# Performance work log

Hardware: AMD Instinct MI355X
Metric: run time of the kernel (lower is better)

Reference implementation:

```python
import jax, jax.numpy as jnp
import numpy as np

EMB = 128
N_TEXT = 80000
N_NODES = 100000
E = 800000
N_REL = 500
PRED_IN = 4 * EMB + 2 * 2 + 2 * 2 * (2 + 2)  # 532


def scatter_mean(x, src, dst, num_nodes):
    # PyG MessagePassing(aggr='mean'): mean of x[src] grouped by dst; empty groups -> 0
    sums = jax.ops.segment_sum(x[src], dst, num_segments=num_nodes)
    cnt = jax.ops.segment_sum(jnp.ones((src.shape[0], 1), x.dtype), dst, num_segments=num_nodes)
    return sums / jnp.maximum(cnt, 1.0)


def setup_inputs() -> dict:
    key = jax.random.key(0)
    ks = jax.random.split(key, 12)
    inp = {
        "h_id_tensor": jax.random.randint(ks[0], (E,), 0, N_NODES),
        "r_id_tensor": jax.random.randint(ks[1], (E,), 0, N_REL),
        "t_id_tensor": jax.random.randint(ks[2], (E,), 0, N_NODES),
        "q_emb": jax.random.normal(ks[3], (1, EMB), jnp.float32),
        "entity_embs": jax.random.normal(ks[4], (N_TEXT, EMB), jnp.float32),
        "num_non_text_entities": N_NODES - N_TEXT,
        "relation_embs": jax.random.normal(ks[5], (N_REL, EMB), jnp.float32),
        "topic_entity_one_hot": jax.random.uniform(ks[6], (N_NODES, 2), jnp.float32),
        # learned params
        "non_text_emb": jax.random.normal(ks[7], (1, EMB), jnp.float32) * 0.02,
        "W1": jax.random.normal(ks[8], (EMB, PRED_IN), jnp.float32) / np.sqrt(PRED_IN),
        "b1": jnp.zeros((EMB,), jnp.float32),
        "W2": jax.random.normal(ks[9], (1, EMB), jnp.float32) / np.sqrt(EMB),
        "b2": jnp.zeros((1,), jnp.float32),
    }
    return inp


def reference(h_id_tensor, r_id_tensor, t_id_tensor, q_emb, entity_embs,
              num_non_text_entities, relation_embs, topic_entity_one_hot,
              non_text_emb, W1, b1, W2, b2):
    num_nodes = entity_embs.shape[0] + num_non_text_entities
    # node embeddings: text entities + shared non-text embedding row
    h_e = jnp.concatenate(
        [entity_embs, jnp.broadcast_to(non_text_emb, (num_non_text_entities, EMB))], axis=0)

    # DDE: forward rounds over (h->t), reverse rounds over (t->h); scatter-mean diffusion
    dde_list = []
    h_pe = topic_entity_one_hot
    for _ in range(2):
        h_pe = scatter_mean(h_pe, h_id_tensor, t_id_tensor, num_nodes)
        dde_list.append(h_pe)
    h_pe_rev = topic_entity_one_hot
    for _ in range(2):
        h_pe_rev = scatter_mean(h_pe_rev, t_id_tensor, h_id_tensor, num_nodes)
        dde_list.append(h_pe_rev)

    h_e_full = jnp.concatenate([h_e, topic_entity_one_hot] + dde_list, axis=1)  # [N, EMB+10]

    h_r = relation_embs[r_id_tensor]                       # [E, EMB]
    h_q = jnp.broadcast_to(q_emb, (h_r.shape[0], EMB))     # [E, EMB]
    h_triple = jnp.concatenate(
        [h_q, h_e_full[h_id_tensor], h_r, h_e_full[t_id_tensor]], axis=1)  # [E, PRED_IN]

    hidden = jax.nn.relu(h_triple @ W1.T + b1)             # [E, EMB]
    pred = hidden @ W2.T + b2                              # [E, 1]
    return pred
```

## Files before the change

kernel.cpp:

```cpp
#include <hip/hip_runtime.h>

#define EMB 128
#define W1LD 532
#define KP 160
#define ST 264
#define BSH 9
#define BNODES 512
#define EPB 8192

typedef unsigned long long u64;
typedef unsigned int u32;
typedef unsigned short u16;
typedef __attribute__((ext_vector_type(8))) short short8;
typedef __attribute__((ext_vector_type(4))) float f32x4;

__device__ __forceinline__ u16 f2bf(float x) {
    unsigned u = __float_as_uint(x);
    unsigned r = (u + 0x7fffu + ((u >> 16) & 1u)) >> 16;
    return (u16)r;
}
__device__ __forceinline__ float bf2f_lo(unsigned u) { return __uint_as_float(u << 16); }
__device__ __forceinline__ float bf2f_hi(unsigned u) { return __uint_as_float(u & 0xffff0000u); }

__global__ __launch_bounds__(1024) void khist(
    const int* __restrict__ h_id, const int* __restrict__ t_id,
    u32* __restrict__ hist, int E, int NBKT, int NSB)
{
    __shared__ u32 lh[512];
    const int t = threadIdx.x, sb = blockIdx.x;
    const int rows = 2 * NBKT;
    if (t < rows) lh[t] = 0;
    __syncthreads();
    const int base = sb * EPB;
#pragma unroll
    for (int c = 0; c < EPB / 1024; c++) {
        int e = base + c * 1024 + t;
        if (e < E) {
            atomicAdd(&lh[t_id[e] >> BSH], 1u);
            atomicAdd(&lh[NBKT + (h_id[e] >> BSH)], 1u);
        }
    }
    __syncthreads();
    if (t < rows) hist[t * NSB + sb] = lh[t];
}

__global__ __launch_bounds__(256) void kscanA(
    u32* __restrict__ hist, u32* __restrict__ tot, int NSB)
{
    __shared__ u32 s[256];
    const int t = threadIdx.x, row = blockIdx.x;
    u32 v = (t < NSB) ? hist[row * NSB + t] : 0;
    s[t] = v;
    __syncthreads();
    for (int o = 1; o < 256; o <<= 1) {
        u32 x = (t >= o) ? s[t - o] : 0;
        __syncthreads();
        s[t] += x;
        __syncthreads();
    }
    if (t < NSB) hist[row * NSB + t] = s[t] - v;
    if (t == 255) tot[row] = s[255];
}

__global__ __launch_bounds__(1024) void kplace(
    const int* __restrict__ h_id, const int* __restrict__ t_id,
    const u32* __restrict__ hist, const u32* __restrict__ tot,
    u32* __restrict__ bstart,
    u32* __restrict__ perm_t, u32* __restrict__ perm_h,
    int E, int NBKT, int NSB)
{
    __shared__ u32 cur[512];
    const int t = threadIdx.x, sb = blockIdx.x;
    const int rows = 2 * NBKT;
    if (t < rows) {
        const int d  = (t < NBKT) ? 1 : 0;
        const int b0 = (t < NBKT) ? 0 : NBKT;
        u32 base = 0;
        for (int b = b0; b < t; b++) base += tot[b];
        cur[t] = base + hist[t * NSB + sb];
        if (sb == 0) {
            const int seg = (t < NBKT) ? 0 : (NBKT + 1);
            bstart[seg + (t - b0)] = base;
            if (t == b0) bstart[seg + NBKT] = (u32)E;
        }
        (void)d;
    }
    __syncthreads();
    const int ebase = sb * EPB;
#pragma unroll
    for (int c = 0; c < EPB / 1024; c++) {
        int e = ebase + c * 1024 + t;
        if (e < E) {
            int tt = t_id[e], h = h_id[e];
            u32 pt = atomicAdd(&cur[tt >> BSH], 1u);
            perm_t[pt] = (u32)h | ((u32)(tt & (BNODES - 1)) << 17);
            u32 ph = atomicAdd(&cur[NBKT + (h >> BSH)], 1u);
            perm_h[ph] = (u32)tt | ((u32)(h & (BNODES - 1)) << 17);
        }
    }
}

template<int ROUND>
__global__ __launch_bounds__(256) void kscat(
    const u32* __restrict__ perm_t, const u32* __restrict__ perm_h,
    const u32* __restrict__ bstart,
    const float* __restrict__ topic,
    const float* __restrict__ src_t, const float* __restrict__ src_h,
    float* __restrict__ out_t, float* __restrict__ out_h,
    const float* __restrict__ W1, const float* __restrict__ q,
    const float* __restrict__ rel, const float* __restrict__ b1,
    u16* __restrict__ WBF, float* __restrict__ qWb, u16* __restrict__ Rbf,
    int N, int NBKT, int NREL)
{
    const int bid = blockIdx.x, t = threadIdx.x;
    if (bid < 2 * NBKT) {
        __shared__ u64 acc[BNODES];
        const int d = (bid < NBKT) ? 0 : 1;
        const int b = bid - d * NBKT;
        const u32* perm = d ? perm_h : perm_t;
        const float* srcv = (ROUND == 1) ? topic : (d ? src_h : src_t);
        float* out = d ? out_h : out_t;

        for (int i = t; i < BNODES; i += 256) acc[i] = 0;
        __syncthreads();
        const u32 s0 = bstart[d * (NBKT + 1) + b];
        const u32 s1 = bstart[d * (NBKT + 1) + b + 1];
        for (u32 i = s0 + t; i < s1; i += 256) {
            u32 rec  = perm[i];
            u32 src  = rec & 0x1FFFFu;
            u32 slot = rec >> 17;
            float2 v = *(const float2*)(srcv + 2 * src);
            u64 p = (u64)__float2uint_rn(v.x * 1048576.0f)
                  | ((u64)__float2uint_rn(v.y * 1048576.0f) << 26)
                  | (1ull << 52);
            atomicAdd(&acc[slot], p);
        }
        __syncthreads();
        for (int i = t; i < BNODES; i += 256) {
            int node = b * BNODES + i;
            if (node < N) {
                u64 a = acc[i];
                float cnt = (float)(u32)(a >> 52);
                float inv = (1.0f / 1048576.0f) / fmaxf(cnt, 1.0f);
                float2 m;
                m.x = (float)(u32)(a & 0x3FFFFFFu) * inv;
                m.y = (float)(u32)((a >> 26) & 0x3FFFFFFu) * inv;
                *(float2*)(out + 2 * node) = m;
            }
        }
        return;
    }
    if (ROUND != 1) return;
    const int pb = bid - 2 * NBKT;
    if (pb < KP) {
        int k = pb, n = t;
        float v = 0.0f;
        if (k < 138) {
            v = (n < 128) ? W1[(size_t)n * W1LD + 128 + k]
                          : W1[(size_t)(n - 128) * W1LD + 394 + k];
        }
        int kstep = k >> 5, quad = (k >> 3) & 3, j = k & 7;
        WBF[(((size_t)(kstep * 4 + quad) * 256 + n) << 3) + j] = f2bf(v);
        return;
    }
    int b = pb - KP;
    __shared__ float v[EMB];
    if (t < EMB) v[t] = (b == 0) ? q[t] : rel[(size_t)(b - 1) * EMB + t];
    __syncthreads();
    if (t < EMB) {
        const float* w = W1 + (size_t)t * W1LD + (b == 0 ? 0 : 266);
        float s = 0.0f;
#pragma unroll
        for (int k = 0; k < EMB; k += 4) {
            float4 wv = *(const float4*)(w + k);
            s += wv.x * v[k] + wv.y * v[k + 1] + wv.z * v[k + 2] + wv.w * v[k + 3];
        }
        if (b == 0) qWb[t] = s + b1[t];
        else        Rbf[(size_t)(b - 1) * EMB + t] = f2bf(s);
    }
}

__global__ __launch_bounds__(256) void k2b_node(
    const float* __restrict__ ent, const float* __restrict__ nte,
    const float* __restrict__ topic,
    const float* __restrict__ dde1f, const float* __restrict__ dde2f,
    const float* __restrict__ dde3f, const float* __restrict__ dde4f,
    const u16* __restrict__ WBF, const float* __restrict__ qWb,
    u16* __restrict__ A, u16* __restrict__ B,
    int NT, int N)
{
    __shared__ __align__(16) u16 lds[32 * ST];
    const int t = threadIdx.x;
    const int lane = t & 63;
    const int w    = t >> 6;
    const int ln15 = lane & 15;
    const int quad = lane >> 4;
    const int m0   = (w & 1) * 16;
    const int n0   = (w >> 1) * 128;
    const int nblk = blockIdx.x * 32;

    {
        int m  = t >> 3;
        int kq = (t & 7) << 4;
        int gn = nblk + m;
        const float* src = (gn < N) ? ((gn < NT) ? ent + (size_t)gn * EMB + kq
                                                 : nte + kq)
                                    : nte;
        u16 pk[16];
#pragma unroll
        for (int p = 0; p < 4; p++) {
            float4 v = (gn < N) ? *(const float4*)(src + 4 * p)
                                : make_float4(0.f, 0.f, 0.f, 0.f);
            pk[4 * p + 0] = f2bf(v.x); pk[4 * p + 1] = f2bf(v.y);
            pk[4 * p + 2] = f2bf(v.z); pk[4 * p + 3] = f2bf(v.w);
        }
        *(uint4*)&lds[m * ST + kq]     = *(uint4*)&pk[0];
        *(uint4*)&lds[m * ST + kq + 8] = *(uint4*)&pk[8];
    }
    if (t < 32) {
        int gn = nblk + t;
        if (gn < N) {
            float2 tp = *(const float2*)(topic + 2 * gn);
            float2 d1 = *(const float2*)(dde1f + 2 * gn);
            float2 d2 = *(const float2*)(dde2f + 2 * gn);
            float2 d3 = *(const float2*)(dde3f + 2 * gn);
            float2 d4 = *(const float2*)(dde4f + 2 * gn);
            lds[t * ST + 128] = f2bf(tp.x); lds[t * ST + 129] = f2bf(tp.y);
            lds[t * ST + 130] = f2bf(d1.x); lds[t * ST + 131] = f2bf(d1.y);
            lds[t * ST + 132] = f2bf(d2.x); lds[t * ST + 133] = f2bf(d2.y);
            lds[t * ST + 134] = f2bf(d3.x); lds[t * ST + 135] = f2bf(d3.y);
            lds[t * ST + 136] = f2bf(d4.x); lds[t * ST + 137] = f2bf(d4.y);
        } else {
#pragma unroll
            for (int z = 128; z < 138; z++) lds[t * ST + z] = 0;
        }
#pragma unroll
        for (int z = 138; z < KP; z++) lds[t * ST + z] = 0;
    }
    __syncthreads();

    f32x4 acc[8];
#pragma unroll
    for (int i = 0; i < 8; i++) acc[i] = (f32x4){0.f, 0.f, 0.f, 0.f};

    const u16* wbbase = WBF + (((size_t)quad * 256 + n0 + ln15) << 3);
#pragma unroll
    for (int ks = 0; ks < 5; ks++) {
        short8 a = *(const short8*)&lds[(m0 + ln15) * ST + ks * 32 + quad * 8];
        const u16* wb = wbbase + ((size_t)ks * 4 * 256 * 8);
#pragma unroll
        for (int nt = 0; nt < 8; nt++) {
            short8 b = *(const short8*)(wb + (nt << 7));
            acc[nt] = __builtin_amdgcn_mfma_f32_16x16x32_bf16(a, b, acc[nt], 0, 0, 0);
        }
    }

    __syncthreads();
#pragma unroll
    for (int nt = 0; nt < 8; nt++) {
        int c = n0 + nt * 16 + ln15;
        float qv = (n0 == 0) ? qWb[c] : 0.0f;
#pragma unroll
        for (int r = 0; r < 4; r++) {
            int row = m0 + quad * 4 + r;
            lds[row * ST + c] = f2bf(acc[nt][r] + qv);
        }
    }
    __syncthreads();
    {
        int m  = t >> 3;
        int c0 = (t & 7) * 32;
        int gn = nblk + m;
        if (gn < N) {
            uint4 v0 = *(uint4*)&lds[m * ST + c0];
            uint4 v1 = *(uint4*)&lds[m * ST + c0 + 8];
            uint4 v2 = *(uint4*)&lds[m * ST + c0 + 16];
            uint4 v3 = *(uint4*)&lds[m * ST + c0 + 24];
            u16* dst = (c0 < 128) ? (A + (size_t)gn * EMB + c0)
                                  : (B + (size_t)gn * EMB + (c0 - 128));
            ((uint4*)dst)[0] = v0;
            ((uint4*)dst)[1] = v1;
            ((uint4*)dst)[2] = v2;
            ((uint4*)dst)[3] = v3;
        }
    }
}

__global__ __launch_bounds__(256) void edge_pred(
    const int* __restrict__ h_id, const int* __restrict__ r_id,
    const int* __restrict__ t_id,
    const u16* __restrict__ A, const u16* __restrict__ B,
    const u16* __restrict__ Rbf,
    const float* __restrict__ W2, const float* __restrict__ b2,
    float* __restrict__ out, int E)
{
    const int t    = threadIdx.x;
    const int lane = t & 63;
    const int g    = lane >> 4;
    const int k    = lane & 15;
    const int wv   = t >> 6;
    const int e    = blockIdx.x * 16 + wv * 4 + g;

    const float4 w0 = *(const float4*)(W2 + k * 8);
    const float4 w1 = *(const float4*)(W2 + k * 8 + 4);

    float s = 0.0f;
    if (e < E) {
        const int h = h_id[e], r = r_id[e], tt = t_id[e];
        const uint4 ua = *(const uint4*)(A + (size_t)h * EMB + k * 8);
        const uint4 ub = *(const uint4*)(B + (size_t)tt * EMB + k * 8);
        const uint4 ur = *(const uint4*)(Rbf + (size_t)r * EMB + k * 8);

        s  = fmaxf(bf2f_lo(ua.x) + bf2f_lo(ur.x) + bf2f_lo(ub.x), 0.0f) * w0.x;
        s += fmaxf(bf2f_hi(ua.x) + bf2f_hi(ur.x) + bf2f_hi(ub.x), 0.0f) * w0.y;
        s += fmaxf(bf2f_lo(ua.y) + bf2f_lo(ur.y) + bf2f_lo(ub.y), 0.0f) * w0.z;
        s += fmaxf(bf2f_hi(ua.y) + bf2f_hi(ur.y) + bf2f_hi(ub.y), 0.0f) * w0.w;
        s += fmaxf(bf2f_lo(ua.z) + bf2f_lo(ur.z) + bf2f_lo(ub.z), 0.0f) * w1.x;
        s += fmaxf(bf2f_hi(ua.z) + bf2f_hi(ur.z) + bf2f_hi(ub.z), 0.0f) * w1.y;
        s += fmaxf(bf2f_lo(ua.w) + bf2f_lo(ur.w) + bf2f_lo(ub.w), 0.0f) * w1.z;
        s += fmaxf(bf2f_hi(ua.w) + bf2f_hi(ur.w) + bf2f_hi(ub.w), 0.0f) * w1.w;
    }
    s += __shfl_xor(s, 1, 64);
    s += __shfl_xor(s, 2, 64);
    s += __shfl_xor(s, 4, 64);
    s += __shfl_xor(s, 8, 64);
    if (k == 0 && e < E) out[e] = s + b2[0];
}


extern "C" void kernel_launch(void* const* d_in, const int* in_sizes, int n_in,
                              void* d_out, int out_size, void* d_ws, size_t ws_size,
                              hipStream_t stream)
{
    const int*   h_id  = (const int*)d_in[0];
    const int*   r_id  = (const int*)d_in[1];
    const int*   t_id  = (const int*)d_in[2];
    const float* q_emb = (const float*)d_in[3];
    const float* ent   = (const float*)d_in[4];
    const float* rel   = (const float*)d_in[6];
    const float* topic = (const float*)d_in[7];
    const float* nte   = (const float*)d_in[8];
    const float* W1    = (const float*)d_in[9];
    const float* b1    = (const float*)d_in[10];
    const float* W2    = (const float*)d_in[11];
    const float* b2    = (const float*)d_in[12];

    const int E    = in_sizes[0];
    const int NT   = in_sizes[4] / EMB;
    const int N    = in_sizes[7] / 2;
    const int NREL = in_sizes[6] / EMB;

    const int NBKT = (N + BNODES - 1) >> BSH;
    const int NSB  = (E + EPB - 1) / EPB;

    float* qWb  = (float*)d_ws;
    u16* Rbf    = (u16*)(qWb + EMB);
    u16* WBF    = Rbf + (size_t)NREL * EMB;
    float* dde1f = (float*)(WBF + (size_t)KP * 256);
    float* dde2f = dde1f + 2 * (size_t)N;
    float* dde3f = dde2f + 2 * (size_t)N;
    float* dde4f = dde3f + 2 * (size_t)N;
    u16* Aw = (u16*)(dde4f + 2 * (size_t)N);
    u16* Bw = Aw + (size_t)N * EMB;

    u32* hist   = (u32*)Aw;
    u32* tot    = hist + (size_t)2 * NBKT * NSB;
    u32* bstart = tot + 2 * NBKT;
    u32* perm_t = bstart + 2 * (NBKT + 1);
    u32* perm_h = perm_t + E;

    const int nn = (N + 31) / 32;

    khist<<<NSB, 1024, 0, stream>>>(h_id, t_id, hist, E, NBKT, NSB);
    kscanA<<<2 * NBKT, 256, 0, stream>>>(hist, tot, NSB);
    kplace<<<NSB, 1024, 0, stream>>>(h_id, t_id, hist, tot, bstart,
                                     perm_t, perm_h, E, NBKT, NSB);

    kscat<1><<<2 * NBKT + KP + 1 + NREL, 256, 0, stream>>>(
        perm_t, perm_h, bstart, topic, nullptr, nullptr, dde1f, dde3f,
        W1, q_emb, rel, b1, WBF, qWb, Rbf, N, NBKT, NREL);

    kscat<2><<<2 * NBKT, 256, 0, stream>>>(
        perm_t, perm_h, bstart, topic, dde1f, dde3f, dde2f, dde4f,
        W1, q_emb, rel, b1, WBF, qWb, Rbf, N, NBKT, NREL);

    k2b_node<<<nn, 256, 0, stream>>>(
        ent, nte, topic, dde1f, dde2f, dde3f, dde4f,
        WBF, qWb, Aw, Bw, NT, N);

    edge_pred<<<(E + 15) / 16, 256, 0, stream>>>(
        h_id, r_id, t_id, Aw, Bw, Rbf, W2, b2, (float*)d_out, E);
}
```

Baseline: 256.3 us.

## Process edges in head-sorted order with packed records and fp16 dot2 epilogue

The placement kernel now writes a 64-bit packed record (h, t, r, original edge id) in head-bucket order, and the edge prediction kernel reads these sorted records. Consecutive edges then share A rows, which improves cache locality, and results are scattered back to their original index. Node and relation projections switch from bf16 to fp16 so the edge epilogue can use packed half adds, max and fdot2. EPB is also halved to get more histogram and placement blocks. Costs are wider perm records, a scattered output write, fp16 range and precision risk, and a fallback path when workspace or size limits fail.

```diff
diff --git a/kernel.cpp b/kernel.cpp
--- a/kernel.cpp
+++ b/kernel.cpp
@@ -6,21 +6,49 @@
 #define ST 264
 #define BSH 9
 #define BNODES 512
-#define EPB 8192
+#define EPB 4096
 
 typedef unsigned long long u64;
 typedef unsigned int u32;
 typedef unsigned short u16;
 typedef __attribute__((ext_vector_type(8))) short short8;
 typedef __attribute__((ext_vector_type(4))) float f32x4;
+typedef _Float16 h2 __attribute__((ext_vector_type(2)));
 
 __device__ __forceinline__ u16 f2bf(float x) {
     unsigned u = __float_as_uint(x);
     unsigned r = (u + 0x7fffu + ((u >> 16) & 1u)) >> 16;
     return (u16)r;
 }
-__device__ __forceinline__ float bf2f_lo(unsigned u) { return __uint_as_float(u << 16); }
-__device__ __forceinline__ float bf2f_hi(unsigned u) { return __uint_as_float(u & 0xffff0000u); }
+__device__ __forceinline__ u16 f2h(float x) {
+    union { _Float16 h; u16 u; } c; c.h = (_Float16)x; return c.u;
+}
+__device__ __forceinline__ h2 u2h(unsigned u) {
+    union { unsigned u; h2 h; } c; c.u = u; return c.h;
+}
+
+__device__ __forceinline__ float ep8(const uint4& ua, const uint4& ub,
+                                     const uint4& ur, const uint4& uw, float s) {
+    const h2 z = {(_Float16)0.0f, (_Float16)0.0f};
+#define EP1(c)                                                         \
+    {                                                                  \
+        h2 x = u2h(ua.c) + u2h(ur.c) + u2h(ub.c);                      \
+        x = __builtin_elementwise_max(x, z);                           \
+        h2 w = u2h(uw.c);                                              \
+        _Pragma("clang diagnostic push")                               \
+        s = FDOT2(x, w, s);                                            \
+        _Pragma("clang diagnostic pop")                                \
+    }
+#if __has_builtin(__builtin_amdgcn_fdot2)
+#define FDOT2(x, w, s) __builtin_amdgcn_fdot2(x, w, s, false)
+#else
+#define FDOT2(x, w, s) (s + (float)x[0] * (float)w[0] + (float)x[1] * (float)w[1])
+#endif
+    EP1(x) EP1(y) EP1(z) EP1(w)
+#undef EP1
+#undef FDOT2
+    return s;
+}
 
 __global__ __launch_bounds__(1024) void khist(
     const int* __restrict__ h_id, const int* __restrict__ t_id,
@@ -63,17 +91,17 @@
 }
 
 __global__ __launch_bounds__(1024) void kplace(
-    const int* __restrict__ h_id, const int* __restrict__ t_id,
+    const int* __restrict__ h_id, const int* __restrict__ r_id,
+    const int* __restrict__ t_id,
     const u32* __restrict__ hist, const u32* __restrict__ tot,
     u32* __restrict__ bstart,
-    u32* __restrict__ perm_t, u32* __restrict__ perm_h,
+    u32* __restrict__ perm_t, u64* __restrict__ perm_e,
     int E, int NBKT, int NSB)
 {
     __shared__ u32 cur[512];
     const int t = threadIdx.x, sb = blockIdx.x;
     const int rows = 2 * NBKT;
     if (t < rows) {
-        const int d  = (t < NBKT) ? 1 : 0;
         const int b0 = (t < NBKT) ? 0 : NBKT;
         u32 base = 0;
         for (int b = b0; b < t; b++) base += tot[b];
@@ -83,7 +111,6 @@
             bstart[seg + (t - b0)] = base;
             if (t == b0) bstart[seg + NBKT] = (u32)E;
         }
-        (void)d;
     }
     __syncthreads();
     const int ebase = sb * EPB;
@@ -91,25 +118,28 @@
     for (int c = 0; c < EPB / 1024; c++) {
         int e = ebase + c * 1024 + t;
         if (e < E) {
-            int tt = t_id[e], h = h_id[e];
+            int tt = t_id[e], h = h_id[e], r = r_id[e];
             u32 pt = atomicAdd(&cur[tt >> BSH], 1u);
             perm_t[pt] = (u32)h | ((u32)(tt & (BNODES - 1)) << 17);
             u32 ph = atomicAdd(&cur[NBKT + (h >> BSH)], 1u);
-            perm_h[ph] = (u32)tt | ((u32)(h & (BNODES - 1)) << 17);
+            perm_e[ph] = (u64)h | ((u64)tt << 17) | ((u64)r << 34)
+                       | ((u64)e << 43);
         }
     }
 }
 
 template<int ROUND>
 __global__ __launch_bounds__(256) void kscat(
-    const u32* __restrict__ perm_t, const u32* __restrict__ perm_h,
+    const u32* __restrict__ perm_t, const u64* __restrict__ perm_e,
     const u32* __restrict__ bstart,
     const float* __restrict__ topic,
     const float* __restrict__ src_t, const float* __restrict__ src_h,
     float* __restrict__ out_t, float* __restrict__ out_h,
     const float* __restrict__ W1, const float* __restrict__ q,
     const float* __restrict__ rel, const float* __restrict__ b1,
-    u16* __restrict__ WBF, float* __restrict__ qWb, u16* __restrict__ Rbf,
+    const float* __restrict__ W2,
+    u16* __restrict__ WBF, float* __restrict__ qWb,
+    u16* __restrict__ W2h, u16* __restrict__ Rbf,
     int N, int NBKT, int NREL)
 {
     const int bid = blockIdx.x, t = threadIdx.x;
@@ -117,7 +147,6 @@
         __shared__ u64 acc[BNODES];
         const int d = (bid < NBKT) ? 0 : 1;
         const int b = bid - d * NBKT;
-        const u32* perm = d ? perm_h : perm_t;
         const float* srcv = (ROUND == 1) ? topic : (d ? src_h : src_t);
         float* out = d ? out_h : out_t;
 
@@ -125,15 +154,28 @@
         __syncthreads();
         const u32 s0 = bstart[d * (NBKT + 1) + b];
         const u32 s1 = bstart[d * (NBKT + 1) + b + 1];
-        for (u32 i = s0 + t; i < s1; i += 256) {
-            u32 rec  = perm[i];
-            u32 src  = rec & 0x1FFFFu;
-            u32 slot = rec >> 17;
-            float2 v = *(const float2*)(srcv + 2 * src);
-            u64 p = (u64)__float2uint_rn(v.x * 1048576.0f)
-                  | ((u64)__float2uint_rn(v.y * 1048576.0f) << 26)
-                  | (1ull << 52);
-            atomicAdd(&acc[slot], p);
+        if (d == 0) {
+            for (u32 i = s0 + t; i < s1; i += 256) {
+                u32 rec  = perm_t[i];
+                u32 src  = rec & 0x1FFFFu;
+                u32 slot = rec >> 17;
+                float2 v = *(const float2*)(srcv + 2 * src);
+                u64 p = (u64)__float2uint_rn(v.x * 1048576.0f)
+                      | ((u64)__float2uint_rn(v.y * 1048576.0f) << 26)
+                      | (1ull << 52);
+                atomicAdd(&acc[slot], p);
+            }
+        } else {
+            for (u32 i = s0 + t; i < s1; i += 256) {
+                u64 rec  = perm_e[i];
+                u32 src  = (u32)(rec >> 17) & 0x1FFFFu;
+                u32 slot = (u32)rec & (BNODES - 1);
+                float2 v = *(const float2*)(srcv + 2 * src);
+                u64 p = (u64)__float2uint_rn(v.x * 1048576.0f)
+                      | ((u64)__float2uint_rn(v.y * 1048576.0f) << 26)
+                      | (1ull << 52);
+                atomicAdd(&acc[slot], p);
+            }
         }
         __syncthreads();
         for (int i = t; i < BNODES; i += 256) {
@@ -175,8 +217,8 @@
             float4 wv = *(const float4*)(w + k);
             s += wv.x * v[k] + wv.y * v[k + 1] + wv.z * v[k + 2] + wv.w * v[k + 3];
         }
-        if (b == 0) qWb[t] = s + b1[t];
-        else        Rbf[(size_t)(b - 1) * EMB + t] = f2bf(s);
+        if (b == 0) { qWb[t] = s + b1[t]; W2h[t] = f2h(W2[t]); }
+        else        Rbf[(size_t)(b - 1) * EMB + t] = f2h(s);
     }
 }
 
@@ -263,7 +305,7 @@
 #pragma unroll
         for (int r = 0; r < 4; r++) {
             int row = m0 + quad * 4 + r;
-            lds[row * ST + c] = f2bf(acc[nt][r] + qv);
+            lds[row * ST + c] = f2h(acc[nt][r] + qv);
         }
     }
     __syncthreads();
@@ -286,13 +328,47 @@
     }
 }
 
-__global__ __launch_bounds__(256) void edge_pred(
+__global__ __launch_bounds__(256) void edge_pred_srt(
+    const u64* __restrict__ perm_e,
+    const u16* __restrict__ A, const u16* __restrict__ B,
+    const u16* __restrict__ Rbf, const u16* __restrict__ W2h,
+    const float* __restrict__ b2, float* __restrict__ out, int E)
+{
+    const int t    = threadIdx.x;
+    const int lane = t & 63;
+    const int g    = lane >> 4;
+    const int k    = lane & 15;
+    const int wv   = t >> 6;
+    const int i    = blockIdx.x * 16 + wv * 4 + g;
+    const bool valid = i < E;
+
+    const uint4 uw = *(const uint4*)(W2h + k * 8);
+    float s = 0.0f;
+    u32 e = 0;
+    if (valid) {
+        u64 rec = perm_e[i];
+        u32 h  = (u32)rec & 0x1FFFFu;
+        u32 tt = (u32)(rec >> 17) & 0x1FFFFu;
+        u32 r  = (u32)(rec >> 34) & 0x1FFu;
+        e = (u32)(rec >> 43);
+        const uint4 ua = *(const uint4*)(A + (size_t)h * EMB + k * 8);
+        const uint4 ub = *(const uint4*)(B + (size_t)tt * EMB + k * 8);
+        const uint4 ur = *(const uint4*)(Rbf + (size_t)r * EMB + k * 8);
+        s = ep8(ua, ub, ur, uw, 0.0f);
+    }
+    s += __shfl_xor(s, 1, 64);
+    s += __shfl_xor(s, 2, 64);
+    s += __shfl_xor(s, 4, 64);
+    s += __shfl_xor(s, 8, 64);
+    if (k == 0 && valid) out[e] = s + b2[0];
+}
+
+__global__ __launch_bounds__(256) void edge_pred_f16(
     const int* __restrict__ h_id, const int* __restrict__ r_id,
     const int* __restrict__ t_id,
     const u16* __restrict__ A, const u16* __restrict__ B,
-    const u16* __restrict__ Rbf,
-    const float* __restrict__ W2, const float* __restrict__ b2,
-    float* __restrict__ out, int E)
+    const u16* __restrict__ Rbf, const u16* __restrict__ W2h,
+    const float* __restrict__ b2, float* __restrict__ out, int E)
 {
     const int t    = threadIdx.x;
     const int lane = t & 63;
@@ -301,24 +377,14 @@
     const int wv   = t >> 6;
     const int e    = blockIdx.x * 16 + wv * 4 + g;
 
-    const float4 w0 = *(const float4*)(W2 + k * 8);
-    const float4 w1 = *(const float4*)(W2 + k * 8 + 4);
-
+    const uint4 uw = *(const uint4*)(W2h + k * 8);
     float s = 0.0f;
     if (e < E) {
         const int h = h_id[e], r = r_id[e], tt = t_id[e];
         const uint4 ua = *(const uint4*)(A + (size_t)h * EMB + k * 8);
         const uint4 ub = *(const uint4*)(B + (size_t)tt * EMB + k * 8);
         const uint4 ur = *(const uint4*)(Rbf + (size_t)r * EMB + k * 8);
-
-        s  = fmaxf(bf2f_lo(ua.x) + bf2f_lo(ur.x) + bf2f_lo(ub.x), 0.0f) * w0.x;
-        s += fmaxf(bf2f_hi(ua.x) + bf2f_hi(ur.x) + bf2f_hi(ub.x), 0.0f) * w0.y;
-        s += fmaxf(bf2f_lo(ua.y) + bf2f_lo(ur.y) + bf2f_lo(ub.y), 0.0f) * w0.z;
-        s += fmaxf(bf2f_hi(ua.y) + bf2f_hi(ur.y) + bf2f_hi(ub.y), 0.0f) * w0.w;
-        s += fmaxf(bf2f_lo(ua.z) + bf2f_lo(ur.z) + bf2f_lo(ub.z), 0.0f) * w1.x;
-        s += fmaxf(bf2f_hi(ua.z) + bf2f_hi(ur.z) + bf2f_hi(ub.z), 0.0f) * w1.y;
-        s += fmaxf(bf2f_lo(ua.w) + bf2f_lo(ur.w) + bf2f_lo(ub.w), 0.0f) * w1.z;
-        s += fmaxf(bf2f_hi(ua.w) + bf2f_hi(ur.w) + bf2f_hi(ub.w), 0.0f) * w1.w;
+        s = ep8(ua, ub, ur, uw, 0.0f);
     }
     s += __shfl_xor(s, 1, 64);
     s += __shfl_xor(s, 2, 64);
@@ -354,7 +420,8 @@
     const int NSB  = (E + EPB - 1) / EPB;
 
     float* qWb  = (float*)d_ws;
-    u16* Rbf    = (u16*)(qWb + EMB);
+    u16* W2h    = (u16*)(qWb + EMB);
+    u16* Rbf    = W2h + EMB;
     u16* WBF    = Rbf + (size_t)NREL * EMB;
     float* dde1f = (float*)(WBF + (size_t)KP * 256);
     float* dde2f = dde1f + 2 * (size_t)N;
@@ -362,32 +429,43 @@
     float* dde4f = dde3f + 2 * (size_t)N;
     u16* Aw = (u16*)(dde4f + 2 * (size_t)N);
     u16* Bw = Aw + (size_t)N * EMB;
+    u64* perm_ded = (u64*)(Bw + (size_t)N * EMB);
 
     u32* hist   = (u32*)Aw;
     u32* tot    = hist + (size_t)2 * NBKT * NSB;
     u32* bstart = tot + 2 * NBKT;
     u32* perm_t = bstart + 2 * (NBKT + 1);
-    u32* perm_h = perm_t + E;
+    u64* perm_alias = (u64*)(((size_t)(perm_t + E) + 7) & ~(size_t)7);
+
+    size_t need_srt = (size_t)((char*)(perm_ded + E) - (char*)d_ws);
+    const bool srt = (ws_size >= need_srt) && (E < (1 << 20)) &&
+                     (N <= (1 << 17)) && (NREL <= (1 << 9)) && (NSB <= 256);
+    u64* perm_e = srt ? perm_ded : perm_alias;
 
     const int nn = (N + 31) / 32;
 
     khist<<<NSB, 1024, 0, stream>>>(h_id, t_id, hist, E, NBKT, NSB);
     kscanA<<<2 * NBKT, 256, 0, stream>>>(hist, tot, NSB);
-    kplace<<<NSB, 1024, 0, stream>>>(h_id, t_id, hist, tot, bstart,
-                                     perm_t, perm_h, E, NBKT, NSB);
+    kplace<<<NSB, 1024, 0, stream>>>(h_id, r_id, t_id, hist, tot, bstart,
+                                     perm_t, perm_e, E, NBKT, NSB);
 
     kscat<1><<<2 * NBKT + KP + 1 + NREL, 256, 0, stream>>>(
-        perm_t, perm_h, bstart, topic, nullptr, nullptr, dde1f, dde3f,
-        W1, q_emb, rel, b1, WBF, qWb, Rbf, N, NBKT, NREL);
+        perm_t, perm_e, bstart, topic, nullptr, nullptr, dde1f, dde3f,
+        W1, q_emb, rel, b1, W2, WBF, qWb, W2h, Rbf, N, NBKT, NREL);
 
     kscat<2><<<2 * NBKT, 256, 0, stream>>>(
-        perm_t, perm_h, bstart, topic, dde1f, dde3f, dde2f, dde4f,
-        W1, q_emb, rel, b1, WBF, qWb, Rbf, N, NBKT, NREL);
+        perm_t, perm_e, bstart, topic, dde1f, dde3f, dde2f, dde4f,
+        W1, q_emb, rel, b1, W2, WBF, qWb, W2h, Rbf, N, NBKT, NREL);
 
     k2b_node<<<nn, 256, 0, stream>>>(
         ent, nte, topic, dde1f, dde2f, dde3f, dde4f,
         WBF, qWb, Aw, Bw, NT, N);
 
-    edge_pred<<<(E + 15) / 16, 256, 0, stream>>>(
-        h_id, r_id, t_id, Aw, Bw, Rbf, W2, b2, (float*)d_out, E);
-}
+    if (srt) {
+        edge_pred_srt<<<(E + 15) / 16, 256, 0, stream>>>(
+            perm_e, Aw, Bw, Rbf, W2h, b2, (float*)d_out, E);
+    } else {
+        edge_pred_f16<<<(E + 15) / 16, 256, 0, stream>>>(
+            h_id, r_id, t_id, Aw, Bw, Rbf, W2h, b2, (float*)d_out, E);
+    }
+}
```

Measured after the change: 249.0 us. 2.8% less time.
